# Kernel optimization log

Measured on AMD Instinct MI355X. Metric: run time of the kernel, lower is better.

The kernel has to match this reference:

```python
import jax, jax.numpy as jnp
import numpy as np

B = 8          # batch
S = 256        # nx+1 = ny+1 grid resolution
N = S * S      # number of DoFs per component
DIM = 2        # output vector dimension (= d_out)
W = 32         # FNO channel width
M1 = 12        # Fourier modes dim 1
M2 = 12        # Fourier modes dim 2
WF = 128       # final MLP hidden width
NL = 4         # number of Fourier layers
PADF = 8       # padding fraction denominator


def setup_inputs() -> dict:
    key = jax.random.key(0)
    ks = jax.random.split(key, 16)
    sc = 1.0 / (W * W)  # torch FNO spectral weight init scale
    return {
        "x": jax.random.normal(ks[0], (B, N), jnp.float32),
        "d2v_in": jax.random.permutation(ks[1], jnp.arange(N)),
        "v2d_out": jax.random.permutation(ks[2], jnp.arange(N)),
        "fc0_w": jax.random.normal(ks[3], (W, 3), jnp.float32) * 0.1,
        "fc0_b": jnp.zeros((W,), jnp.float32),
        "spec_w1r": jax.random.uniform(ks[4], (NL, W, W, M1, M2), jnp.float32) * sc,
        "spec_w1i": jax.random.uniform(ks[5], (NL, W, W, M1, M2), jnp.float32) * sc,
        "spec_w2r": jax.random.uniform(ks[6], (NL, W, W, M1, M2), jnp.float32) * sc,
        "spec_w2i": jax.random.uniform(ks[7], (NL, W, W, M1, M2), jnp.float32) * sc,
        "conv_w": jax.random.normal(ks[8], (NL, W, W), jnp.float32) * 0.05,
        "conv_b": jnp.zeros((NL, W), jnp.float32),
        "mlp_w1": jax.random.normal(ks[9], (WF, W), jnp.float32) * 0.05,
        "mlp_b1": jnp.zeros((WF,), jnp.float32),
        "mlp_w2": jax.random.normal(ks[10], (DIM, WF), jnp.float32) * 0.05,
        "mlp_b2": jnp.zeros((DIM,), jnp.float32),
    }


def _speconv(x, w1, w2):
    # x: (B, C, H, Wd) real; w1/w2: (C_in, C_out, M1, M2) complex64
    Bh, C, H, Wd = x.shape
    xft = jnp.fft.rfft2(x)  # (B, C, H, Wd//2+1)
    o1 = jnp.einsum('bixy,ioxy->boxy', xft[:, :, :M1, :M2], w1)
    o2 = jnp.einsum('bixy,ioxy->boxy', xft[:, :, -M1:, :M2], w2)
    out_ft = jnp.zeros((Bh, C, H, Wd // 2 + 1), jnp.complex64)
    out_ft = out_ft.at[:, :, :M1, :M2].set(o1).at[:, :, -M1:, :M2].set(o2)
    return jnp.fft.irfft2(out_ft, s=(H, Wd))


def reference(x, d2v_in, v2d_out, fc0_w, fc0_b,
              spec_w1r, spec_w1i, spec_w2r, spec_w2i,
              conv_w, conv_b, mlp_w1, mlp_b1, mlp_w2, mlp_b2):
    # DoF -> vertex gather and lift to image
    xg = x[:, d2v_in].reshape(B, 1, S, S)
    h = jnp.transpose(xg, (0, 2, 3, 1))  # (B, S, S, 1)
    # append normalized grid coordinates (get_grid2d)
    g = jnp.linspace(0.0, 1.0, S, dtype=jnp.float32)
    grid = jnp.stack(jnp.meshgrid(g, g, indexing='ij'), axis=-1)  # (S, S, 2)
    grid = jnp.broadcast_to(grid[None], (B, S, S, 2))
    h = jnp.concatenate([h, grid], axis=-1)
    # fc0 lifting
    h = h @ fc0_w.T + fc0_b              # (B, S, S, W)
    h = jnp.transpose(h, (0, 3, 1, 2))   # (B, W, S, S)
    # zero pad (non-periodic domain)
    p = S // PADF
    h = jnp.pad(h, ((0, 0), (0, 0), (0, p), (0, p)))  # (B, W, S+p, S+p)
    w1 = (spec_w1r + 1j * spec_w1i).astype(jnp.complex64)
    w2 = (spec_w2r + 1j * spec_w2i).astype(jnp.complex64)
    for l in range(NL):
        sp = _speconv(h, w1[l], w2[l])
        cv = jnp.einsum('bchw,oc->bohw', h, conv_w[l]) + conv_b[l][None, :, None, None]
        h = cv + sp
        if l != NL - 1:
            h = jax.nn.gelu(h, approximate=False)  # torch GELU default = exact erf
    # crop padding (s_outputspace=None path)
    h = h[..., :S, :S]
    # final two-layer MLP projection
    h = jnp.transpose(h, (0, 2, 3, 1))  # (B, S, S, W)
    h = jax.nn.gelu(h @ mlp_w1.T + mlp_b1, approximate=False) @ mlp_w2.T + mlp_b2
    h = jnp.transpose(h, (0, 3, 1, 2)).reshape(B, DIM, -1)  # (B, DIM, N)
    # vertex -> DoF scatter/gather and interleave components
    out = h[:, :, v2d_out]              # (B, DIM, N)
    out = jnp.transpose(out, (0, 2, 1)).reshape(B, -1)  # (B, N*DIM)
    return out
```

## Files before the change

kernel.cpp:

```cpp
#include <hip/hip_runtime.h>
#include <math.h>

#define S    256
#define Hp   288
#define C    32
#define KY   12
#define NK   24
#define Bn   8
#define PI_D 3.14159265358979323846264338327950288

#define SZ_TW  (NK*Hp*2)
#define OFF_TW 0
#define OFF_TWT (OFF_TW + SZ_TW)
#define SZ_TWT (Hp*KY*2)
#define OFF_H  (OFF_TWT + SZ_TWT)
#define SZ_H   (Bn*C*Hp*Hp)
#define OFF_Y  (OFF_H + SZ_H)
#define SZ_Y   (Bn*C*Hp*KY*2)
#define OFF_X  (OFF_Y + SZ_Y)
#define SZ_X   (Bn*C*NK*KY*2)
#define OFF_O  (OFF_X + 2*SZ_X)
#define SZ_O   SZ_X
#define OFF_Z  (OFF_O + SZ_O)
#define SZ_Z   (Bn*Hp*C*KY*2)
#define OFF_T  (OFF_Z + SZ_Z)
#define SZ_T   (Bn*S*S*2)

#define GELU(v) (0.5f*(v)*(1.0f+erff((v)*0.70710678118654752f)))
#define SCHED_FENCE() __builtin_amdgcn_sched_barrier(0)

__global__ void k_tw(float* __restrict__ tw, float* __restrict__ twT) {
    int i = blockIdx.x * 256 + threadIdx.x;
    if (i >= NK * Hp) return;
    int k = i / Hp, xx = i % Hp;
    int f = (k < KY) ? k : (k + 264);
    int m = (f * xx) % Hp;
    double th = (2.0 * PI_D * (double)m) / (double)Hp;
    float c = (float)cos(th), s = (float)sin(th);
    tw[2 * i] = c; tw[2 * i + 1] = s;
    if (k < KY) { twT[xx * 24 + 2 * k] = c; twT[xx * 24 + 2 * k + 1] = s; }
}

__device__ __forceinline__ void rot_tc(float* tc, const float* rk) {
    #pragma unroll
    for (int k = 1; k < 12; ++k) {
        float c0 = tc[2*k], s0 = tc[2*k+1];
        tc[2*k]   = c0 * rk[2*k]   - s0 * rk[2*k+1];
        tc[2*k+1] = c0 * rk[2*k+1] + s0 * rk[2*k];
    }
}

__global__ __launch_bounds__(256, 1) void k_embed(
        const float* __restrict__ xin, const int* __restrict__ d2v,
        const float* __restrict__ fw, const float* __restrict__ fb,
        const float* __restrict__ twT, float* __restrict__ h, float* __restrict__ Y) {
    __shared__ __align__(16) float xs[256];
    __shared__ __align__(16) float YP[3072];
    int x = blockIdx.x, b = blockIdx.y, tid = threadIdx.x;
    size_t rowbase = (size_t)b * 2654208 + (size_t)x * 288;
    if (x >= S) {
        for (int i = tid; i < 32 * 72; i += 256) {
            int c = i / 72, q = i % 72;
            *(float4*)&h[rowbase + (size_t)c * 82944 + q * 4] = make_float4(0, 0, 0, 0);
        }
        for (int i = tid; i < 768; i += 256)
            Y[((size_t)(b * 32 + i / 24) * 288 + x) * 24 + (i % 24)] = 0.f;
        return;
    }
    xs[tid] = xin[b * 65536 + d2v[x * 256 + tid]];
    int o = tid & 31, g = tid >> 5;
    float w0 = fw[o * 3], w1 = fw[o * 3 + 1], w2 = fw[o * 3 + 2], bb = fb[o];
    float gx = x * (1.0f / 255.0f);
    float rk[24];
    #pragma unroll
    for (int q = 0; q < 6; ++q) *(float4*)&rk[4 * q] = *(const float4*)&twT[24 + 4 * q];
    __syncthreads();
    float pr[12], pi[12];
    #pragma unroll
    for (int k = 0; k < 12; ++k) { pr[k] = 0.f; pi[k] = 0.f; }
    #pragma unroll 1
    for (int c3 = 0; c3 < 3; ++c3) {
        int ybase = g * 36 + c3 * 12;
        float tc[24];
        {
            const float* tg = twT + ybase * 24;
            #pragma unroll
            for (int q = 0; q < 6; ++q) *(float4*)&tc[4 * q] = *(const float4*)&tg[4 * q];
        }
        float acc[12];
        #pragma unroll
        for (int j = 0; j < 12; ++j) {
            int y = ybase + j;
            acc[j] = (y < S) ? (w0 * xs[y < S ? y : 0] + w1 * gx + w2 * (y * (1.0f / 255.0f)) + bb) : 0.f;
        }
        float* hw = h + rowbase + (size_t)o * 82944 + ybase;
        #pragma unroll
        for (int q = 0; q < 3; ++q)
            *(float4*)&hw[4 * q] = make_float4(acc[4*q], acc[4*q+1], acc[4*q+2], acc[4*q+3]);
        SCHED_FENCE();
        #pragma unroll
        for (int j = 0; j < 12; ++j) {
            float v = acc[j];
            pr[0] += v;
            #pragma unroll
            for (int k = 1; k < 12; ++k) { pr[k] += v * tc[2 * k]; pi[k] -= v * tc[2 * k + 1]; }
            if (j < 11) rot_tc(tc, rk);
        }
        SCHED_FENCE();
    }
    #pragma unroll
    for (int k = 0; k < 12; ++k) { pr[k] += __shfl_xor(pr[k], 32); pi[k] += __shfl_xor(pi[k], 32); }
    if ((tid & 32) == 0) {
        float* dst = YP + ((tid >> 6) * 32 + o) * 24;
        #pragma unroll
        for (int k = 0; k < 12; ++k) { dst[2 * k] = pr[k]; dst[2 * k + 1] = pi[k]; }
    }
    __syncthreads();
    for (int i = tid; i < 768; i += 256) {
        float s = YP[i] + YP[768 + i] + YP[1536 + i] + YP[2304 + i];
        Y[((size_t)(b * 32 + i / 24) * 288 + x) * 24 + (i % 24)] = s;
    }
}

__global__ __launch_bounds__(288) void k_dftx(const float* __restrict__ Y,
                                              const float* __restrict__ tw,
                                              float* __restrict__ X) {
    __shared__ __align__(16) float Ys[144 * 24];
    int c = blockIdx.x, b = blockIdx.y, half = blockIdx.z, tid = threadIdx.x;
    const float* Yb = Y + (size_t)(b * 32 + c) * 6912 + half * 3456;
    for (int i = tid; i < 864; i += 288)
        *(float4*)&Ys[4 * i] = *(const float4*)&Yb[4 * i];
    __syncthreads();
    int k = tid / 12, ky = tid % 12;
    const float* twk = tw + k * 576 + half * 288;
    float xr = 0.f, xi = 0.f;
    #pragma unroll 4
    for (int xx = 0; xx < 144; ++xx) {
        float yr = Ys[xx * 24 + 2 * ky], yi = Ys[xx * 24 + 2 * ky + 1];
        float cc = twk[2 * xx], ss = twk[2 * xx + 1];
        xr += yr * cc + yi * ss;
        xi += yi * cc - yr * ss;
    }
    size_t oo = (size_t)half * SZ_X + ((size_t)(b * 32 + c) * 288 + tid) * 2;
    X[oo] = xr; X[oo + 1] = xi;
}

__global__ void k_spec(const float* __restrict__ X,
                       const float* __restrict__ w1r, const float* __restrict__ w1i,
                       const float* __restrict__ w2r, const float* __restrict__ w2i,
                       float* __restrict__ O, int l) {
    int t = blockIdx.x * 256 + threadIdx.x;
    int ky = t % KY; int k = (t / KY) % NK; int o = (t / (NK * KY)) % C; int b = t / (C * NK * KY);
    int kk = (k < KY) ? k : (k - KY);
    const float* wr = (k < KY) ? w1r : w2r;
    const float* wi = (k < KY) ? w1i : w2i;
    size_t wbase = (size_t)l * C * C * 144 + (size_t)o * 144 + kk * 12 + ky;
    size_t xbase = (size_t)b * C * NK * KY * 2 + (k * KY + ky) * 2;
    float ar = 0.f, ai = 0.f;
    #pragma unroll 8
    for (int i = 0; i < C; ++i) {
        size_t xo = xbase + (size_t)i * NK * KY * 2;
        float xr = X[xo]     + X[SZ_X + xo];
        float xi = X[xo + 1] + X[SZ_X + xo + 1];
        float wrr = wr[wbase + (size_t)i * C * 144];
        float wii = wi[wbase + (size_t)i * C * 144];
        ar += xr * wrr - xi * wii;
        ai += xr * wii + xi * wrr;
    }
    size_t oo = (((size_t)b * C + o) * NK * KY + k * KY + ky) * 2;
    O[oo] = ar; O[oo + 1] = ai;
}

__global__ __launch_bounds__(384) void k_idftx(const float* __restrict__ O,
                                               const float* __restrict__ tw,
                                               float* __restrict__ Z) {
    int x0 = blockIdx.x * 32; int c = blockIdx.y, b = blockIdx.z;
    int row = threadIdx.x & 31, ky = threadIdx.x >> 5;
    int x = x0 + row;
    const float* Ob = O + ((size_t)(b * C + c)) * NK * KY * 2 + ky * 2;
    float zr = 0.f, zi = 0.f;
    #pragma unroll
    for (int k = 0; k < NK; ++k) {
        float orr = Ob[k * KY * 2], oii = Ob[k * KY * 2 + 1];
        float cc = tw[(k * Hp + x) * 2], ss = tw[(k * Hp + x) * 2 + 1];
        zr += orr * cc - oii * ss;
        zi += orr * ss + oii * cc;
    }
    size_t o = ((((size_t)b * Hp + x) * C + c) * KY + ky) * 2;
    Z[o] = zr; Z[o + 1] = zi;
}

__global__ __launch_bounds__(256, 1) void k_conv(
        float* __restrict__ h, const float* __restrict__ Z,
        const float* __restrict__ cw, const float* __restrict__ cb,
        const float* __restrict__ twT, float* __restrict__ Y,
        int l, int flags) {
    __shared__ __align__(16) float hs[32 * 288];
    __shared__ __align__(16) float cws[32 * 33];
    int x = blockIdx.x, b = blockIdx.y, tid = threadIdx.x;
    int o = tid & 31, g = tid >> 5;
    size_t rowbase = (size_t)b * 2654208 + (size_t)x * 288;
    const float* hb = h + rowbase;
    for (int i = tid; i < 32 * 72; i += 256)
        *(float4*)&hs[4 * i] = *(const float4*)&hb[(size_t)(i / 72) * 82944 + (i % 72) * 4];
    for (int i = tid; i < 1024; i += 256)
        cws[(i >> 5) * 33 + (i & 31)] = cw[l * 1024 + i];
    float rk[24];
    #pragma unroll
    for (int q = 0; q < 6; ++q) *(float4*)&rk[4 * q] = *(const float4*)&twT[24 + 4 * q];
    const float* Zr = Z + ((size_t)(b * 288 + x) * 32 + o) * 24;
    float zr[12], zi[12];
    #pragma unroll
    for (int q = 0; q < 6; ++q) {
        float4 zv = *(const float4*)&Zr[4 * q];
        zr[2*q] = zv.x; zi[2*q] = zv.y; zr[2*q+1] = zv.z; zi[2*q+1] = zv.w;
    }
    float bias = cb[l * 32 + o];
    float pr[12], pi[12];
    #pragma unroll
    for (int k = 0; k < 12; ++k) { pr[k] = 0.f; pi[k] = 0.f; }
    const int gelu_f = flags & 1, wy = flags & 2;
    __syncthreads();
    #pragma unroll 1
    for (int c3 = 0; c3 < 3; ++c3) {
        int ybase = g * 36 + c3 * 12;
        float tc[24];
        {
            const float* tg = twT + ybase * 24;
            #pragma unroll
            for (int q = 0; q < 6; ++q) *(float4*)&tc[4 * q] = *(const float4*)&tg[4 * q];
        }
        float acc[12];
        #pragma unroll
        for (int j = 0; j < 12; ++j) acc[j] = bias;
        #pragma unroll 8
        for (int c = 0; c < 32; ++c) {
            float w = cws[o * 33 + c];
            const float* hr = &hs[c * 288 + ybase];
            float4 h0 = *(const float4*)&hr[0];
            float4 h1 = *(const float4*)&hr[4];
            float4 h2 = *(const float4*)&hr[8];
            acc[0] += h0.x * w; acc[1] += h0.y * w; acc[2]  += h0.z * w; acc[3]  += h0.w * w;
            acc[4] += h1.x * w; acc[5] += h1.y * w; acc[6]  += h1.z * w; acc[7]  += h1.w * w;
            acc[8] += h2.x * w; acc[9] += h2.y * w; acc[10] += h2.z * w; acc[11] += h2.w * w;
        }
        SCHED_FENCE();
        #pragma unroll
        for (int j = 0; j < 12; ++j) {
            float sE = 0.f, sO = 0.f;
            #pragma unroll
            for (int k = 1; k < 12; ++k) {
                float t = zr[k] * tc[2 * k] - zi[k] * tc[2 * k + 1];
                if (k & 1) sO += t; else sE += t;
            }
            float sp = zr[0] + 2.f * (sE + sO);
            float val = acc[j] + sp * (1.0f / 82944.0f);
            if (gelu_f) val = GELU(val);
            acc[j] = val;
            if (wy) {
                pr[0] += val;
                #pragma unroll
                for (int k = 1; k < 12; ++k) { pr[k] += val * tc[2*k]; pi[k] -= val * tc[2*k+1]; }
            }
            if (j < 11) rot_tc(tc, rk);
        }
        SCHED_FENCE();
        float* hw = h + rowbase + (size_t)o * 82944 + ybase;
        #pragma unroll
        for (int q = 0; q < 3; ++q)
            *(float4*)&hw[4 * q] = make_float4(acc[4*q], acc[4*q+1], acc[4*q+2], acc[4*q+3]);
        SCHED_FENCE();
    }
    if (wy) {
        #pragma unroll
        for (int k = 0; k < 12; ++k) { pr[k] += __shfl_xor(pr[k], 32); pi[k] += __shfl_xor(pi[k], 32); }
        __syncthreads();
        float* YP = hs;
        if ((tid & 32) == 0) {
            float* dst = YP + ((tid >> 6) * 32 + o) * 24;
            #pragma unroll
            for (int k = 0; k < 12; ++k) { dst[2 * k] = pr[k]; dst[2 * k + 1] = pi[k]; }
        }
        __syncthreads();
        for (int i = tid; i < 768; i += 256) {
            float s = YP[i] + YP[768 + i] + YP[1536 + i] + YP[2304 + i];
            Y[((size_t)(b * 32 + i / 24) * 288 + x) * 24 + (i % 24)] = s;
        }
    }
}

__global__ __launch_bounds__(256) void k_mlp(const float* __restrict__ h,
                                             const float* __restrict__ w1, const float* __restrict__ b1,
                                             const float* __restrict__ w2, const float* __restrict__ b2,
                                             float* __restrict__ tmp) {
    int bid = blockIdx.x;
    int b = bid >> 7;
    int x = ((bid & 127) << 1) + (threadIdx.x >> 7);
    int lane = threadIdx.x & 127;
    const float* hb = h + (size_t)b * 2654208 + (size_t)x * 288;
    float hc0[32], hc1[32];
    #pragma unroll
    for (int c = 0; c < 32; ++c) {
        hc0[c] = hb[(size_t)c * 82944 + lane];
        hc1[c] = hb[(size_t)c * 82944 + lane + 128];
    }
    float o00 = 0.f, o01 = 0.f, o10 = 0.f, o11 = 0.f;
    for (int f = 0; f < 128; ++f) {
        float a0 = b1[f], a1 = a0;
        #pragma unroll
        for (int c = 0; c < 32; ++c) {
            float w = w1[f * 32 + c];
            a0 += hc0[c] * w; a1 += hc1[c] * w;
        }
        float wa = w2[f], wb = w2[128 + f];
        float g0 = GELU(a0), g1 = GELU(a1);
        o00 += g0 * wa; o01 += g0 * wb;
        o10 += g1 * wa; o11 += g1 * wb;
    }
    float bb0 = b2[0], bb1 = b2[1];
    int p0 = x * 256 + lane;
    size_t base = (size_t)b * 65536;
    *(float2*)&tmp[(base + p0) * 2]       = make_float2(o00 + bb0, o01 + bb1);
    *(float2*)&tmp[(base + p0 + 128) * 2] = make_float2(o10 + bb0, o11 + bb1);
}

__global__ void k_scatter(const float* __restrict__ tmp, const int* __restrict__ v2d,
                          float* __restrict__ out) {
    int id = blockIdx.x * 256 + threadIdx.x;
    int b = id >> 16; int j = id & 65535;
    int p = v2d[j];
    const float2 v = *(const float2*)(tmp + ((size_t)(b << 16) + p) * 2);
    *(float2*)(out + (size_t)id * 2) = v;
}

extern "C" void kernel_launch(void* const* d_in, const int* in_sizes, int n_in,
                              void* d_out, int out_size, void* d_ws, size_t ws_size,
                              hipStream_t stream) {
    const float* xin   = (const float*)d_in[0];
    const int*   d2v   = (const int*)  d_in[1];
    const int*   v2d   = (const int*)  d_in[2];
    const float* fc0w  = (const float*)d_in[3];
    const float* fc0b  = (const float*)d_in[4];
    const float* w1r   = (const float*)d_in[5];
    const float* w1i   = (const float*)d_in[6];
    const float* w2r   = (const float*)d_in[7];
    const float* w2i   = (const float*)d_in[8];
    const float* cw    = (const float*)d_in[9];
    const float* cb    = (const float*)d_in[10];
    const float* mw1   = (const float*)d_in[11];
    const float* mb1   = (const float*)d_in[12];
    const float* mw2   = (const float*)d_in[13];
    const float* mb2   = (const float*)d_in[14];

    float* ws  = (float*)d_ws;
    float* TW  = ws + OFF_TW;
    float* TWT = ws + OFF_TWT;
    float* H   = ws + OFF_H;
    float* Y   = ws + OFF_Y;
    float* X   = ws + OFF_X;
    float* O   = ws + OFF_O;
    float* Z   = ws + OFF_Z;
    float* T   = ws + OFF_T;

    k_tw<<<(NK * Hp + 255) / 256, 256, 0, stream>>>(TW, TWT);
    k_embed<<<dim3(Hp, Bn), 256, 0, stream>>>(xin, d2v, fc0w, fc0b, TWT, H, Y);

    for (int l = 0; l < 4; ++l) {
        k_dftx<<<dim3(32, Bn, 2), 288, 0, stream>>>(Y, TW, X);
        k_spec<<<(Bn * C * NK * KY) / 256, 256, 0, stream>>>(X, w1r, w1i, w2r, w2i, O, l);
        k_idftx<<<dim3(9, 32, Bn), 384, 0, stream>>>(O, TW, Z);
        k_conv<<<dim3(Hp, Bn), 256, 0, stream>>>(H, Z, cw, cb, TWT, Y, l, (l != 3) ? 3 : 0);
    }

    k_mlp<<<1024, 256, 0, stream>>>(H, mw1, mb1, mw2, mb2, T);
    k_scatter<<<(Bn * S * S) / 256, 256, 0, stream>>>(T, v2d, (float*)d_out);
}
```

Before: 847.4 us.

## Halve conv LDS tile by splitting channels, cache half twiddle table in LDS

k_conv now stages the input row in two halves of 16 channels. It holds 36 accumulators in registers across both passes, which halves the hs shared buffer. The twiddle rotation recurrence is replaced by a 144-row twiddle table loaded into shared memory. The upper half of y is handled by a sign-flip symmetry (HI template) instead of rotating twiddles. This cuts LDS footprint and serial rotation dependencies, at the cost of extra syncs, more register pressure and a second global load phase.

Measured after the change: 966.4 us. 14.0% more time.

```diff
diff --git a/kernel.cpp b/kernel.cpp
--- a/kernel.cpp
+++ b/kernel.cpp
@@ -190,24 +190,56 @@
     Z[o] = zr; Z[o + 1] = zi;
 }
 
+template<bool HI>
+__device__ __forceinline__ void epi12(const float* __restrict__ twh, int rb,
+                                      float* acc, const float* zr, const float* zi,
+                                      float* pr, float* pi, int gelu_f, int wy) {
+    #pragma unroll
+    for (int j = 0; j < 12; ++j) {
+        const float* tg = twh + (rb + j) * 24;
+        float tc[24];
+        #pragma unroll
+        for (int q = 0; q < 6; ++q) *(float4*)&tc[4 * q] = *(const float4*)&tg[4 * q];
+        float sE = 0.f, sO = 0.f;
+        #pragma unroll
+        for (int k = 1; k < 12; ++k) {
+            float t = zr[k] * tc[2 * k] - zi[k] * tc[2 * k + 1];
+            if (k & 1) sO += t; else sE += t;
+        }
+        float sp = zr[0] + (HI ? 2.f * (sE - sO) : 2.f * (sE + sO));
+        float val = acc[j] + sp * (1.0f / 82944.0f);
+        if (gelu_f) val = GELU(val);
+        acc[j] = val;
+        if (wy) {
+            pr[0] += val;
+            #pragma unroll
+            for (int k = 1; k < 12; ++k) {
+                float vk = (HI && (k & 1)) ? -val : val;
+                pr[k] += vk * tc[2 * k]; pi[k] -= vk * tc[2 * k + 1];
+            }
+        }
+        if (j & 1) SCHED_FENCE();
+    }
+}
+
 __global__ __launch_bounds__(256, 1) void k_conv(
         float* __restrict__ h, const float* __restrict__ Z,
         const float* __restrict__ cw, const float* __restrict__ cb,
         const float* __restrict__ twT, float* __restrict__ Y,
         int l, int flags) {
-    __shared__ __align__(16) float hs[32 * 288];
+    __shared__ __align__(16) float hs[16 * 288];
+    __shared__ __align__(16) float twh[144 * 24];
     __shared__ __align__(16) float cws[32 * 33];
     int x = blockIdx.x, b = blockIdx.y, tid = threadIdx.x;
     int o = tid & 31, g = tid >> 5;
     size_t rowbase = (size_t)b * 2654208 + (size_t)x * 288;
     const float* hb = h + rowbase;
-    for (int i = tid; i < 32 * 72; i += 256)
-        *(float4*)&hs[4 * i] = *(const float4*)&hb[(size_t)(i / 72) * 82944 + (i % 72) * 4];
+    for (int i = tid; i < 864; i += 256)
+        *(float4*)&twh[4 * i] = *(const float4*)&twT[4 * i];
     for (int i = tid; i < 1024; i += 256)
         cws[(i >> 5) * 33 + (i & 31)] = cw[l * 1024 + i];
-    float rk[24];
-    #pragma unroll
-    for (int q = 0; q < 6; ++q) *(float4*)&rk[4 * q] = *(const float4*)&twT[24 + 4 * q];
+    for (int i = tid; i < 1152; i += 256)
+        *(float4*)&hs[4 * i] = *(const float4*)&hb[(size_t)(i / 72) * 82944 + (i % 72) * 4];
     const float* Zr = Z + ((size_t)(b * 288 + x) * 32 + o) * 24;
     float zr[12], zi[12];
     #pragma unroll
@@ -220,55 +252,53 @@
     #pragma unroll
     for (int k = 0; k < 12; ++k) { pr[k] = 0.f; pi[k] = 0.f; }
     const int gelu_f = flags & 1, wy = flags & 2;
+    float acc[36];
+    #pragma unroll
+    for (int j = 0; j < 36; ++j) acc[j] = bias;
     __syncthreads();
     #pragma unroll 1
     for (int c3 = 0; c3 < 3; ++c3) {
         int ybase = g * 36 + c3 * 12;
-        float tc[24];
-        {
-            const float* tg = twT + ybase * 24;
-            #pragma unroll
-            for (int q = 0; q < 6; ++q) *(float4*)&tc[4 * q] = *(const float4*)&tg[4 * q];
-        }
-        float acc[12];
-        #pragma unroll
-        for (int j = 0; j < 12; ++j) acc[j] = bias;
+        float* a = acc + c3 * 12;
         #pragma unroll 8
-        for (int c = 0; c < 32; ++c) {
+        for (int c = 0; c < 16; ++c) {
             float w = cws[o * 33 + c];
             const float* hr = &hs[c * 288 + ybase];
             float4 h0 = *(const float4*)&hr[0];
             float4 h1 = *(const float4*)&hr[4];
             float4 h2 = *(const float4*)&hr[8];
-            acc[0] += h0.x * w; acc[1] += h0.y * w; acc[2]  += h0.z * w; acc[3]  += h0.w * w;
-            acc[4] += h1.x * w; acc[5] += h1.y * w; acc[6]  += h1.z * w; acc[7]  += h1.w * w;
-            acc[8] += h2.x * w; acc[9] += h2.y * w; acc[10] += h2.z * w; acc[11] += h2.w * w;
+            a[0] += h0.x * w; a[1]  += h0.y * w; a[2]  += h0.z * w; a[3]  += h0.w * w;
+            a[4] += h1.x * w; a[5]  += h1.y * w; a[6]  += h1.z * w; a[7]  += h1.w * w;
+            a[8] += h2.x * w; a[9]  += h2.y * w; a[10] += h2.z * w; a[11] += h2.w * w;
         }
         SCHED_FENCE();
-        #pragma unroll
-        for (int j = 0; j < 12; ++j) {
-            float sE = 0.f, sO = 0.f;
-            #pragma unroll
-            for (int k = 1; k < 12; ++k) {
-                float t = zr[k] * tc[2 * k] - zi[k] * tc[2 * k + 1];
-                if (k & 1) sO += t; else sE += t;
-            }
-            float sp = zr[0] + 2.f * (sE + sO);
-            float val = acc[j] + sp * (1.0f / 82944.0f);
-            if (gelu_f) val = GELU(val);
-            acc[j] = val;
-            if (wy) {
-                pr[0] += val;
-                #pragma unroll
-                for (int k = 1; k < 12; ++k) { pr[k] += val * tc[2*k]; pi[k] -= val * tc[2*k+1]; }
-            }
-            if (j < 11) rot_tc(tc, rk);
+    }
+    __syncthreads();
+    for (int i = tid; i < 1152; i += 256)
+        *(float4*)&hs[4 * i] = *(const float4*)&hb[(size_t)(16 + i / 72) * 82944 + (i % 72) * 4];
+    __syncthreads();
+    #pragma unroll 1
+    for (int c3 = 0; c3 < 3; ++c3) {
+        int ybase = g * 36 + c3 * 12;
+        float* a = acc + c3 * 12;
+        #pragma unroll 8
+        for (int c = 0; c < 16; ++c) {
+            float w = cws[o * 33 + 16 + c];
+            const float* hr = &hs[c * 288 + ybase];
+            float4 h0 = *(const float4*)&hr[0];
+            float4 h1 = *(const float4*)&hr[4];
+            float4 h2 = *(const float4*)&hr[8];
+            a[0] += h0.x * w; a[1]  += h0.y * w; a[2]  += h0.z * w; a[3]  += h0.w * w;
+            a[4] += h1.x * w; a[5]  += h1.y * w; a[6]  += h1.z * w; a[7]  += h1.w * w;
+            a[8] += h2.x * w; a[9]  += h2.y * w; a[10] += h2.z * w; a[11] += h2.w * w;
         }
         SCHED_FENCE();
+        if (g < 4) epi12<false>(twh, ybase,       a, zr, zi, pr, pi, gelu_f, wy);
+        else       epi12<true >(twh, ybase - 144, a, zr, zi, pr, pi, gelu_f, wy);
         float* hw = h + rowbase + (size_t)o * 82944 + ybase;
         #pragma unroll
         for (int q = 0; q < 3; ++q)
-            *(float4*)&hw[4 * q] = make_float4(acc[4*q], acc[4*q+1], acc[4*q+2], acc[4*q+3]);
+            *(float4*)&hw[4 * q] = make_float4(a[4*q], a[4*q+1], a[4*q+2], a[4*q+3]);
         SCHED_FENCE();
     }
     if (wy) {
```

## Replace twiddle rotation with quarter-period symmetry lookup from shared memory

Applied to the files above, without the earlier changes.

The twiddle recurrence (rot_tc) in the conv epilogue is replaced by loading exact twiddles for the first 72 rows from shared memory. The other rows are derived through quarter-period symmetry, using a compile-time quadrant index Q selected per wave pair via a switch. The conv weight tile is also stored transposed in shared memory so threads read consecutive addresses without padding. This removes the serial complex-multiply chain and its rounding drift, at the cost of more LDS reads per output column and four template instantiations that enlarge code size.

Measured after the change: 835.5 us. About the same (-1.4%).

```diff
diff --git a/kernel.cpp b/kernel.cpp
--- a/kernel.cpp
+++ b/kernel.cpp
@@ -190,52 +190,64 @@
     Z[o] = zr; Z[o + 1] = zi;
 }
 
-__global__ __launch_bounds__(256, 1) void k_conv(
-        float* __restrict__ h, const float* __restrict__ Z,
-        const float* __restrict__ cw, const float* __restrict__ cb,
-        const float* __restrict__ twT, float* __restrict__ Y,
-        int l, int flags) {
-    __shared__ __align__(16) float hs[32 * 288];
-    __shared__ __align__(16) float cws[32 * 33];
-    int x = blockIdx.x, b = blockIdx.y, tid = threadIdx.x;
-    int o = tid & 31, g = tid >> 5;
-    size_t rowbase = (size_t)b * 2654208 + (size_t)x * 288;
-    const float* hb = h + rowbase;
-    for (int i = tid; i < 32 * 72; i += 256)
-        *(float4*)&hs[4 * i] = *(const float4*)&hb[(size_t)(i / 72) * 82944 + (i % 72) * 4];
-    for (int i = tid; i < 1024; i += 256)
-        cws[(i >> 5) * 33 + (i & 31)] = cw[l * 1024 + i];
-    float rk[24];
-    #pragma unroll
-    for (int q = 0; q < 6; ++q) *(float4*)&rk[4 * q] = *(const float4*)&twT[24 + 4 * q];
-    const float* Zr = Z + ((size_t)(b * 288 + x) * 32 + o) * 24;
-    float zr[12], zi[12];
-    #pragma unroll
-    for (int q = 0; q < 6; ++q) {
-        float4 zv = *(const float4*)&Zr[4 * q];
-        zr[2*q] = zv.x; zi[2*q] = zv.y; zr[2*q+1] = zv.z; zi[2*q+1] = zv.w;
-    }
-    float bias = cb[l * 32 + o];
-    float pr[12], pi[12];
-    #pragma unroll
-    for (int k = 0; k < 12; ++k) { pr[k] = 0.f; pi[k] = 0.f; }
-    const int gelu_f = flags & 1, wy = flags & 2;
-    __syncthreads();
+template<int Q>
+__device__ __forceinline__ void epi12(const float* __restrict__ twq, int rowq,
+                                      float* acc, const float* zr, const float* zi,
+                                      float* pr, float* pi, int gelu_f, int wy) {
+    #pragma unroll
+    for (int j = 0; j < 12; ++j) {
+        const float* tg = twq + (rowq + j) * 24;
+        float tc[24];
+        #pragma unroll
+        for (int q = 0; q < 6; ++q) *(float4*)&tc[4 * q] = *(const float4*)&tg[4 * q];
+        float sA = 0.f, sB = 0.f;
+        #pragma unroll
+        for (int k = 1; k < 12; ++k) {
+            const int e = (k * Q) & 3;
+            float c = tc[2 * k], s = tc[2 * k + 1];
+            float t;
+            if      (e == 0) t =  zr[k] * c - zi[k] * s;
+            else if (e == 1) t = -zr[k] * s - zi[k] * c;
+            else if (e == 2) t = -zr[k] * c + zi[k] * s;
+            else             t =  zr[k] * s + zi[k] * c;
+            if (k & 1) sB += t; else sA += t;
+        }
+        float sp = zr[0] + 2.f * (sA + sB);
+        float val = acc[j] + sp * (1.0f / 82944.0f);
+        if (gelu_f) val = GELU(val);
+        acc[j] = val;
+        if (wy) {
+            pr[0] += val;
+            #pragma unroll
+            for (int k = 1; k < 12; ++k) {
+                const int e = (k * Q) & 3;
+                float c = tc[2 * k], s = tc[2 * k + 1];
+                if      (e == 0) { pr[k] += val * c; pi[k] -= val * s; }
+                else if (e == 1) { pr[k] -= val * s; pi[k] -= val * c; }
+                else if (e == 2) { pr[k] -= val * c; pi[k] += val * s; }
+                else             { pr[k] += val * s; pi[k] += val * c; }
+            }
+        }
+        if (j & 1) SCHED_FENCE();
+    }
+}
+
+template<int Q>
+__device__ __forceinline__ void conv_body(
+        const float* __restrict__ hs, const float* __restrict__ twq,
+        const float* __restrict__ cwsT, float* __restrict__ h, size_t rowbase,
+        int o, int g, float bias, const float* zr, const float* zi,
+        float* pr, float* pi, int gelu_f, int wy) {
     #pragma unroll 1
     for (int c3 = 0; c3 < 3; ++c3) {
         int ybase = g * 36 + c3 * 12;
-        float tc[24];
-        {
-            const float* tg = twT + ybase * 24;
-            #pragma unroll
-            for (int q = 0; q < 6; ++q) *(float4*)&tc[4 * q] = *(const float4*)&tg[4 * q];
-        }
+        int rowq  = (g & 1) * 36 + c3 * 12;
         float acc[12];
         #pragma unroll
         for (int j = 0; j < 12; ++j) acc[j] = bias;
         #pragma unroll 8
         for (int c = 0; c < 32; ++c) {
-            float w = cws[o * 33 + c];
+            float w = cwsT[c * 32 + o];
             const float* hr = &hs[c * 288 + ybase];
             float4 h0 = *(const float4*)&hr[0];
             float4 h1 = *(const float4*)&hr[4];
@@ -245,31 +257,51 @@
             acc[8] += h2.x * w; acc[9] += h2.y * w; acc[10] += h2.z * w; acc[11] += h2.w * w;
         }
         SCHED_FENCE();
-        #pragma unroll
-        for (int j = 0; j < 12; ++j) {
-            float sE = 0.f, sO = 0.f;
-            #pragma unroll
-            for (int k = 1; k < 12; ++k) {
-                float t = zr[k] * tc[2 * k] - zi[k] * tc[2 * k + 1];
-                if (k & 1) sO += t; else sE += t;
-            }
-            float sp = zr[0] + 2.f * (sE + sO);
-            float val = acc[j] + sp * (1.0f / 82944.0f);
-            if (gelu_f) val = GELU(val);
-            acc[j] = val;
-            if (wy) {
-                pr[0] += val;
-                #pragma unroll
-                for (int k = 1; k < 12; ++k) { pr[k] += val * tc[2*k]; pi[k] -= val * tc[2*k+1]; }
-            }
-            if (j < 11) rot_tc(tc, rk);
-        }
-        SCHED_FENCE();
+        epi12<Q>(twq, rowq, acc, zr, zi, pr, pi, gelu_f, wy);
         float* hw = h + rowbase + (size_t)o * 82944 + ybase;
         #pragma unroll
         for (int q = 0; q < 3; ++q)
             *(float4*)&hw[4 * q] = make_float4(acc[4*q], acc[4*q+1], acc[4*q+2], acc[4*q+3]);
         SCHED_FENCE();
+    }
+}
+
+__global__ __launch_bounds__(256, 1) void k_conv(
+        float* __restrict__ h, const float* __restrict__ Z,
+        const float* __restrict__ cw, const float* __restrict__ cb,
+        const float* __restrict__ twT, float* __restrict__ Y,
+        int l, int flags) {
+    __shared__ __align__(16) float hs[32 * 288];
+    __shared__ __align__(16) float twq[72 * 24];
+    __shared__ __align__(16) float cwsT[1024];
+    int x = blockIdx.x, b = blockIdx.y, tid = threadIdx.x;
+    int o = tid & 31, g = tid >> 5;
+    size_t rowbase = (size_t)b * 2654208 + (size_t)x * 288;
+    const float* hb = h + rowbase;
+    for (int i = tid; i < 432; i += 256)
+        *(float4*)&twq[4 * i] = *(const float4*)&twT[4 * i];
+    for (int i = tid; i < 1024; i += 256)
+        cwsT[i] = cw[l * 1024 + (i & 31) * 32 + (i >> 5)];
+    for (int i = tid; i < 2304; i += 256)
+        *(float4*)&hs[4 * i] = *(const float4*)&hb[(size_t)(i / 72) * 82944 + (i % 72) * 4];
+    const float* Zr = Z + ((size_t)(b * 288 + x) * 32 + o) * 24;
+    float zr[12], zi[12];
+    #pragma unroll
+    for (int q = 0; q < 6; ++q) {
+        float4 zv = *(const float4*)&Zr[4 * q];
+        zr[2*q] = zv.x; zi[2*q] = zv.y; zr[2*q+1] = zv.z; zi[2*q+1] = zv.w;
+    }
+    float bias = cb[l * 32 + o];
+    float pr[12], pi[12];
+    #pragma unroll
+    for (int k = 0; k < 12; ++k) { pr[k] = 0.f; pi[k] = 0.f; }
+    const int gelu_f = flags & 1, wy = flags & 2;
+    __syncthreads();
+    switch (tid >> 6) {
+        case 0: conv_body<0>(hs, twq, cwsT, h, rowbase, o, g, bias, zr, zi, pr, pi, gelu_f, wy); break;
+        case 1: conv_body<1>(hs, twq, cwsT, h, rowbase, o, g, bias, zr, zi, pr, pi, gelu_f, wy); break;
+        case 2: conv_body<2>(hs, twq, cwsT, h, rowbase, o, g, bias, zr, zi, pr, pi, gelu_f, wy); break;
+        default: conv_body<3>(hs, twq, cwsT, h, rowbase, o, g, bias, zr, zi, pr, pi, gelu_f, wy); break;
     }
     if (wy) {
         #pragma unroll
```

## Exploit twiddle symmetry to pair low/high y columns in conv epilogue

Applied to the files above, without the earlier changes.

Restructures k_conv to 384 threads, each handling a pair of columns y and y+144. The DFT twiddles for the paired column are derived from the low one through quarter-period phase symmetry (even/odd k sign flips), which halves the trig evaluations. Twiddles now come from an LDS-staged table instead of incremental rotation, and the Y reduction sums six partial groups. This adds registers (al/ah accumulators) and more threads per block, so occupancy and register pressure could shift.

After: 931.9 us. 10.0% more time.

```diff
diff --git a/kernel.cpp b/kernel.cpp
--- a/kernel.cpp
+++ b/kernel.cpp
@@ -190,24 +190,71 @@
     Z[o] = zr; Z[o + 1] = zi;
 }
 
-__global__ __launch_bounds__(256, 1) void k_conv(
+template<int QP>
+__device__ __forceinline__ void epi_pairs(const float* __restrict__ twq, int rowq,
+                                          float* al, float* ah,
+                                          const float* zr, const float* zi,
+                                          float* pr, float* pi, int gelu_f, int wy) {
+    #pragma unroll
+    for (int j = 0; j < 12; ++j) {
+        const float* tg = twq + (rowq + j) * 24;
+        float tc[24];
+        #pragma unroll
+        for (int q = 0; q < 6; ++q) *(float4*)&tc[4 * q] = *(const float4*)&tg[4 * q];
+        float SAE = 0.f, SAO = 0.f;
+        #pragma unroll
+        for (int k = 1; k < 12; ++k) {
+            const int e = (k * QP) & 3;
+            float c = tc[2 * k], s = tc[2 * k + 1];
+            float A;
+            if      (e == 0) A =  zr[k] * c - zi[k] * s;
+            else if (e == 1) A = -zr[k] * s - zi[k] * c;
+            else if (e == 2) A = -zr[k] * c + zi[k] * s;
+            else             A =  zr[k] * s + zi[k] * c;
+            if (k & 1) SAO += A; else SAE += A;
+        }
+        float spl = zr[0] + 2.f * (SAE + SAO);
+        float sph = zr[0] + 2.f * (SAE - SAO);
+        float vl = al[j] + spl * (1.0f / 82944.0f);
+        float vh = ah[j] + sph * (1.0f / 82944.0f);
+        if (gelu_f) { vl = GELU(vl); vh = GELU(vh); }
+        al[j] = vl; ah[j] = vh;
+        if (wy) {
+            float u = vl + vh, v = vl - vh;
+            pr[0] += u;
+            #pragma unroll
+            for (int k = 1; k < 12; ++k) {
+                const int e = (k * QP) & 3;
+                float c = tc[2 * k], s = tc[2 * k + 1];
+                float w_ = (k & 1) ? v : u;
+                if      (e == 0) { pr[k] += w_ * c; pi[k] -= w_ * s; }
+                else if (e == 1) { pr[k] -= w_ * s; pi[k] -= w_ * c; }
+                else if (e == 2) { pr[k] -= w_ * c; pi[k] += w_ * s; }
+                else             { pr[k] += w_ * s; pi[k] += w_ * c; }
+            }
+        }
+        SCHED_FENCE();
+    }
+}
+
+__global__ __launch_bounds__(384, 1) void k_conv(
         float* __restrict__ h, const float* __restrict__ Z,
         const float* __restrict__ cw, const float* __restrict__ cb,
         const float* __restrict__ twT, float* __restrict__ Y,
         int l, int flags) {
-    __shared__ __align__(16) float hs[32 * 288];
+    __shared__ __align__(16) float hs[9216];
+    __shared__ __align__(16) float twq[1728];
     __shared__ __align__(16) float cws[32 * 33];
     int x = blockIdx.x, b = blockIdx.y, tid = threadIdx.x;
     int o = tid & 31, g = tid >> 5;
     size_t rowbase = (size_t)b * 2654208 + (size_t)x * 288;
     const float* hb = h + rowbase;
-    for (int i = tid; i < 32 * 72; i += 256)
+    for (int i = tid; i < 432; i += 384)
+        *(float4*)&twq[4 * i] = *(const float4*)&twT[4 * i];
+    for (int i = tid; i < 1024; i += 384)
+        cws[(i >> 5) * 33 + (i & 31)] = cw[l * 1024 + i];
+    for (int i = tid; i < 2304; i += 384)
         *(float4*)&hs[4 * i] = *(const float4*)&hb[(size_t)(i / 72) * 82944 + (i % 72) * 4];
-    for (int i = tid; i < 1024; i += 256)
-        cws[(i >> 5) * 33 + (i & 31)] = cw[l * 1024 + i];
-    float rk[24];
-    #pragma unroll
-    for (int q = 0; q < 6; ++q) *(float4*)&rk[4 * q] = *(const float4*)&twT[24 + 4 * q];
     const float* Zr = Z + ((size_t)(b * 288 + x) * 32 + o) * 24;
     float zr[12], zi[12];
     #pragma unroll
@@ -221,55 +268,35 @@
     for (int k = 0; k < 12; ++k) { pr[k] = 0.f; pi[k] = 0.f; }
     const int gelu_f = flags & 1, wy = flags & 2;
     __syncthreads();
-    #pragma unroll 1
-    for (int c3 = 0; c3 < 3; ++c3) {
-        int ybase = g * 36 + c3 * 12;
-        float tc[24];
-        {
-            const float* tg = twT + ybase * 24;
-            #pragma unroll
-            for (int q = 0; q < 6; ++q) *(float4*)&tc[4 * q] = *(const float4*)&tg[4 * q];
-        }
-        float acc[12];
-        #pragma unroll
-        for (int j = 0; j < 12; ++j) acc[j] = bias;
-        #pragma unroll 8
-        for (int c = 0; c < 32; ++c) {
-            float w = cws[o * 33 + c];
-            const float* hr = &hs[c * 288 + ybase];
-            float4 h0 = *(const float4*)&hr[0];
-            float4 h1 = *(const float4*)&hr[4];
-            float4 h2 = *(const float4*)&hr[8];
-            acc[0] += h0.x * w; acc[1] += h0.y * w; acc[2]  += h0.z * w; acc[3]  += h0.w * w;
-            acc[4] += h1.x * w; acc[5] += h1.y * w; acc[6]  += h1.z * w; acc[7]  += h1.w * w;
-            acc[8] += h2.x * w; acc[9] += h2.y * w; acc[10] += h2.z * w; acc[11] += h2.w * w;
-        }
-        SCHED_FENCE();
-        #pragma unroll
-        for (int j = 0; j < 12; ++j) {
-            float sE = 0.f, sO = 0.f;
-            #pragma unroll
-            for (int k = 1; k < 12; ++k) {
-                float t = zr[k] * tc[2 * k] - zi[k] * tc[2 * k + 1];
-                if (k & 1) sO += t; else sE += t;
-            }
-            float sp = zr[0] + 2.f * (sE + sO);
-            float val = acc[j] + sp * (1.0f / 82944.0f);
-            if (gelu_f) val = GELU(val);
-            acc[j] = val;
-            if (wy) {
-                pr[0] += val;
-                #pragma unroll
-                for (int k = 1; k < 12; ++k) { pr[k] += val * tc[2*k]; pi[k] -= val * tc[2*k+1]; }
-            }
-            if (j < 11) rot_tc(tc, rk);
-        }
-        SCHED_FENCE();
-        float* hw = h + rowbase + (size_t)o * 82944 + ybase;
-        #pragma unroll
-        for (int q = 0; q < 3; ++q)
-            *(float4*)&hw[4 * q] = make_float4(acc[4*q], acc[4*q+1], acc[4*q+2], acc[4*q+3]);
-        SCHED_FENCE();
+    const int yb = g * 12;
+    float al[12], ah[12];
+    #pragma unroll
+    for (int j = 0; j < 12; ++j) { al[j] = bias; ah[j] = bias; }
+    #pragma unroll 8
+    for (int c = 0; c < 32; ++c) {
+        float w = cws[o * 33 + c];
+        const float* hr = &hs[c * 288 + yb];
+        float4 l0 = *(const float4*)&hr[0];
+        float4 l1 = *(const float4*)&hr[4];
+        float4 l2 = *(const float4*)&hr[8];
+        float4 h0 = *(const float4*)&hr[144];
+        float4 h1 = *(const float4*)&hr[148];
+        float4 h2 = *(const float4*)&hr[152];
+        al[0] += l0.x * w; al[1] += l0.y * w; al[2]  += l0.z * w; al[3]  += l0.w * w;
+        al[4] += l1.x * w; al[5] += l1.y * w; al[6]  += l1.z * w; al[7]  += l1.w * w;
+        al[8] += l2.x * w; al[9] += l2.y * w; al[10] += l2.z * w; al[11] += l2.w * w;
+        ah[0] += h0.x * w; ah[1] += h0.y * w; ah[2]  += h0.z * w; ah[3]  += h0.w * w;
+        ah[4] += h1.x * w; ah[5] += h1.y * w; ah[6]  += h1.z * w; ah[7]  += h1.w * w;
+        ah[8] += h2.x * w; ah[9] += h2.y * w; ah[10] += h2.z * w; ah[11] += h2.w * w;
+    }
+    SCHED_FENCE();
+    if (g < 6) epi_pairs<0>(twq, yb,      al, ah, zr, zi, pr, pi, gelu_f, wy);
+    else       epi_pairs<1>(twq, yb - 72, al, ah, zr, zi, pr, pi, gelu_f, wy);
+    float* hw = h + rowbase + (size_t)o * 82944 + yb;
+    #pragma unroll
+    for (int q = 0; q < 3; ++q) {
+        *(float4*)&hw[4 * q]       = make_float4(al[4*q], al[4*q+1], al[4*q+2], al[4*q+3]);
+        *(float4*)&hw[144 + 4 * q] = make_float4(ah[4*q], ah[4*q+1], ah[4*q+2], ah[4*q+3]);
     }
     if (wy) {
         #pragma unroll
@@ -282,8 +309,9 @@
             for (int k = 0; k < 12; ++k) { dst[2 * k] = pr[k]; dst[2 * k + 1] = pi[k]; }
         }
         __syncthreads();
-        for (int i = tid; i < 768; i += 256) {
-            float s = YP[i] + YP[768 + i] + YP[1536 + i] + YP[2304 + i];
+        for (int i = tid; i < 768; i += 384) {
+            float s = YP[i] + YP[768 + i] + YP[1536 + i] + YP[2304 + i]
+                    + YP[3072 + i] + YP[3840 + i];
             Y[((size_t)(b * 32 + i / 24) * 288 + x) * 24 + (i % 24)] = s;
         }
     }
@@ -369,7 +397,7 @@
         k_dftx<<<dim3(32, Bn, 2), 288, 0, stream>>>(Y, TW, X);
         k_spec<<<(Bn * C * NK * KY) / 256, 256, 0, stream>>>(X, w1r, w1i, w2r, w2i, O, l);
         k_idftx<<<dim3(9, 32, Bn), 384, 0, stream>>>(O, TW, Z);
-        k_conv<<<dim3(Hp, Bn), 256, 0, stream>>>(H, Z, cw, cb, TWT, Y, l, (l != 3) ? 3 : 0);
+        k_conv<<<dim3(Hp, Bn), 384, 0, stream>>>(H, Z, cw, cb, TWT, Y, l, (l != 3) ? 3 : 0);
     }
 
     k_mlp<<<1024, 256, 0, stream>>>(H, mw1, mb1, mw2, mb2, T);
```
